# Performance work log

Measured on AMD Instinct MI355X. Metric: run time of the kernel, lower is better.

## Reference

```python
import jax, jax.numpy as jnp
import numpy as np
from jax import lax

K = 15            # contrast_kernel
BRIGHT_T = 0.7    # brightness_threshold

def _box_filter(x, k):
    # x: [B,1,H,W]; uniform k x k conv with SAME (zero) padding, matching F.conv2d(padding=k//2)
    kernel = jnp.full((1, 1, k, k), 1.0 / (k * k), dtype=x.dtype)
    pad = k // 2
    return lax.conv_general_dilated(
        x, kernel, window_strides=(1, 1), padding=[(pad, pad), (pad, pad)],
        dimension_numbers=('NCHW', 'OIHW', 'NCHW'))

def _avg_pool_5x5(x):
    # avg_pool2d(kernel=5, stride=1, padding=2), count_include_pad=True (torch default)
    s = lax.reduce_window(x, jnp.array(0.0, x.dtype), lax.add,
                          window_dimensions=(1, 1, 5, 5), window_strides=(1, 1, 1, 1),
                          padding=[(0, 0), (0, 0), (2, 2), (2, 2)])
    return s / jnp.array(25.0, x.dtype)

def setup_inputs() -> dict:
    key = jax.random.key(0)
    img = jax.random.uniform(key, (16, 3, 1024, 1024), dtype=jnp.float32)
    return {"img": img}

def reference(img) -> jnp.ndarray:
    # luminance: [B,1,H,W]
    lum = (0.299 * img[:, 0:1] + 0.587 * img[:, 1:2] + 0.114 * img[:, 2:3])
    brightness_mask = jax.nn.sigmoid((lum - BRIGHT_T) * 10.0)
    local_mean = _box_filter(lum, K)
    local_var = _box_filter((lum - local_mean) ** 2, K)
    contrast_mask = jax.nn.sigmoid(local_var * 50.0 - 0.5)
    max_rgb = jnp.max(img, axis=1, keepdims=True)
    min_rgb = jnp.min(img, axis=1, keepdims=True)
    saturation = (max_rgb - min_rgb) / (max_rgb + 1e-8)
    low_sat_mask = jax.nn.sigmoid((0.3 - saturation) * 10.0)
    combined = jnp.clip(brightness_mask + 0.5 * contrast_mask * low_sat_mask, 0.0, 1.0)
    return _avg_pool_5x5(combined)
```

## Files before the change

kernel.cpp:

```cpp
#include <hip/hip_runtime.h>


#define BLOCK 512
typedef unsigned short u16;
typedef unsigned int u32;
typedef __attribute__((ext_vector_type(2))) float f32x2;

#define SL 104
#define S1 88

__device__ __forceinline__ float blo(u32 u){ return __uint_as_float(u << 16); }
__device__ __forceinline__ float bhi(u32 u){ return __uint_as_float(u & 0xffff0000u); }
__device__ __forceinline__ u32 pk2(float lo, float hi){
    u32 r; asm("v_cvt_pk_bf16_f32 %0, %1, %2" : "=v"(r) : "v"(lo), "v"(hi)); return r;
}
__device__ __forceinline__ f32x2 pka(f32x2 a, f32x2 b){
    f32x2 d; asm("v_pk_add_f32 %0, %1, %2" : "=v"(d) : "v"(a), "v"(b)); return d;
}
__device__ __forceinline__ f32x2 up2(u32 u){
    f32x2 r; r.x = __uint_as_float(u << 16); r.y = __uint_as_float(u & 0xffff0000u); return r;
}
__device__ __forceinline__ float sigf(float x){ return 1.f / (1.f + __expf(-x)); }
__device__ __forceinline__ float clamp01(float x){ return fminf(fmaxf(x, 0.f), 1.f); }
__device__ __forceinline__ void unp8(uint4 v, float* o){
    o[0]=blo(v.x); o[1]=bhi(v.x); o[2]=blo(v.y); o[3]=bhi(v.y);
    o[4]=blo(v.z); o[5]=bhi(v.z); o[6]=blo(v.w); o[7]=bhi(v.w);
}
__device__ __forceinline__ float satm(float r_, float g_, float b_){
    float mx = fmaxf(r_, fmaxf(g_, b_));
    float mn = fminf(r_, fminf(g_, b_));
    float sat = (mx - mn) / (mx + 1e-8f);
    return sigf((0.3f - sat) * 10.f);
}

template<bool EDGE>
__device__ __forceinline__ void body(const float* __restrict__ pR,
                                     const float* __restrict__ pG,
                                     const float* __restrict__ pB,
                                     float* __restrict__ po,
                                     int oy, int ox, int tid,
                                     u16* sLum, u16* sT1, u16* sDC)
{
    const float C225 = 1.f / 225.f;
    const float CF   = 50.f / 225.f;

    for (int task = tid; task < 96 * 6; task += BLOCK) {
        int r = task / 6, c = task - r * 6;
        int gy = oy - 16 + r;
        int gxb = ox - 16 + 16 * c;
        u32 pk[8];
        #pragma unroll
        for (int sq = 0; sq < 4; ++sq) {
            int gx = gxb + 4 * sq;
            float l0 = 0.f, l1 = 0.f, l2 = 0.f, l3 = 0.f;
            if (!EDGE || ((unsigned)gy < 1024u && (unsigned)gx < 1024u)) {
                int idx = gy * 1024 + gx;
                float4 R  = *(const float4*)&pR[idx];
                float4 G  = *(const float4*)&pG[idx];
                float4 Bc = *(const float4*)&pB[idx];
                l0 = fmaf(0.299f, R.x, fmaf(0.587f, G.x, 0.114f * Bc.x));
                l1 = fmaf(0.299f, R.y, fmaf(0.587f, G.y, 0.114f * Bc.y));
                l2 = fmaf(0.299f, R.z, fmaf(0.587f, G.z, 0.114f * Bc.z));
                l3 = fmaf(0.299f, R.w, fmaf(0.587f, G.w, 0.114f * Bc.w));
            }
            pk[2 * sq]     = pk2(l0, l1);
            pk[2 * sq + 1] = pk2(l2, l3);
        }
        u16* dst = &sLum[r * SL + 16 * c];
        *(uint4*)dst     = make_uint4(pk[0], pk[1], pk[2], pk[3]);
        *(uint4*)(dst+8) = make_uint4(pk[4], pk[5], pk[6], pk[7]);
    }
    __syncthreads();

    for (int task = tid; task < 96 * 6; task += BLOCK) {
        int r = task / 6, g = task - r * 6;
        int s0 = 16 * g;
        const u16* lr = &sLum[r * SL + s0];
        float lv[32];
        unp8(*(const uint4*)lr,        lv);
        unp8(*(const uint4*)(lr + 8),  lv + 8);
        unp8(*(const uint4*)(lr + 16), lv + 16);
        unp8(*(const uint4*)(lr + 24), lv + 24);
        float o[16];
        float s = 0.f;
        #pragma unroll
        for (int k = 0; k < 15; ++k) s += lv[k];
        o[0] = s;
        #pragma unroll
        for (int j = 1; j < 16; ++j) { s += lv[j + 14] - lv[j - 1]; o[j] = s; }
        u16* dst = &sT1[r * S1 + s0];
        if (g < 5) {
            *(uint4*)dst     = make_uint4(pk2(o[0],o[1]), pk2(o[2],o[3]),
                                          pk2(o[4],o[5]), pk2(o[6],o[7]));
            *(uint4*)(dst+8) = make_uint4(pk2(o[8],o[9]),  pk2(o[10],o[11]),
                                          pk2(o[12],o[13]),pk2(o[14],o[15]));
        } else {
            *(uint2*)dst = make_uint2(pk2(o[0],o[1]), pk2(o[2],o[3]));
        }
    }
    __syncthreads();

    for (int task = tid; task < 451; task += BLOCK) {
        int rg = task / 11, cg = task - rg * 11;
        int r0 = 2 * rg, c0 = 8 * cg;
        const u16* hp = &sT1[r0 * S1 + c0];
        f32x2 a0, a1, a2, a3, cs0, cs1, cs2, cs3;
        {
            uint4 v = *(const uint4*)hp;
            a0 = up2(v.x); a1 = up2(v.y); a2 = up2(v.z); a3 = up2(v.w);
        }
        {
            uint4 v = *(const uint4*)(hp + S1);
            cs0 = up2(v.x); cs1 = up2(v.y); cs2 = up2(v.z); cs3 = up2(v.w);
        }
        #pragma unroll
        for (int k = 2; k <= 14; ++k) {
            uint4 v = *(const uint4*)(hp + k * S1);
            cs0 = pka(cs0, up2(v.x)); cs1 = pka(cs1, up2(v.y));
            cs2 = pka(cs2, up2(v.z)); cs3 = pka(cs3, up2(v.w));
        }
        auto emitD = [&](int row, f32x2 t0, f32x2 t1, f32x2 t2, f32x2 t3) {
            const u16* lrow = &sLum[(row + 7) * SL + c0];
            u32 aw  = *(const u32*)(lrow + 6);
            uint4 bv = *(const uint4*)(lrow + 8);
            float L0 = bhi(aw);
            float L1 = blo(bv.x), L2 = bhi(bv.x);
            float L3 = blo(bv.y), L4 = bhi(bv.y);
            float L5 = blo(bv.z), L6 = bhi(bv.z);
            float L7 = blo(bv.w);
            float t_0 = fmaf(-C225, t0.x, L0), t_1 = fmaf(-C225, t0.y, L1);
            float t_2 = fmaf(-C225, t1.x, L2), t_3 = fmaf(-C225, t1.y, L3);
            float t_4 = fmaf(-C225, t2.x, L4), t_5 = fmaf(-C225, t2.y, L5);
            float t_6 = fmaf(-C225, t3.x, L6), t_7 = fmaf(-C225, t3.y, L7);
            float d0=t_0*t_0, d1=t_1*t_1, d2=t_2*t_2, d3=t_3*t_3;
            float d4=t_4*t_4, d5=t_5*t_5, d6=t_6*t_6, d7=t_7*t_7;
            if (EDGE) {
                int gy = oy - 9 + row, gx = ox - 9 + c0;
                bool vy = (unsigned)gy < 1024u;
                d0 = (vy && (unsigned)(gx    ) < 1024u) ? d0 : 0.f;
                d1 = (vy && (unsigned)(gx + 1) < 1024u) ? d1 : 0.f;
                d2 = (vy && (unsigned)(gx + 2) < 1024u) ? d2 : 0.f;
                d3 = (vy && (unsigned)(gx + 3) < 1024u) ? d3 : 0.f;
                d4 = (vy && (unsigned)(gx + 4) < 1024u) ? d4 : 0.f;
                d5 = (vy && (unsigned)(gx + 5) < 1024u) ? d5 : 0.f;
                d6 = (vy && (unsigned)(gx + 6) < 1024u) ? d6 : 0.f;
                d7 = (vy && (unsigned)(gx + 7) < 1024u) ? d7 : 0.f;
            }
            *(uint4*)&sDC[row * S1 + c0] =
                make_uint4(pk2(d0,d1), pk2(d2,d3), pk2(d4,d5), pk2(d6,d7));
        };
        emitD(r0, pka(cs0,a0), pka(cs1,a1), pka(cs2,a2), pka(cs3,a3));
        {
            uint4 v = *(const uint4*)(hp + 15 * S1);
            emitD(r0 + 1, pka(cs0, up2(v.x)), pka(cs1, up2(v.y)),
                          pka(cs2, up2(v.z)), pka(cs3, up2(v.w)));
        }
    }
    __syncthreads();

    for (int task = tid; task < 82 * 5; task += BLOCK) {
        int r = task / 5, g = task - r * 5;
        int s0 = 16 * g;
        const u16* dr = &sDC[r * S1 + s0];
        float lv[32];
        unp8(*(const uint4*)dr,        lv);
        unp8(*(const uint4*)(dr + 8),  lv + 8);
        unp8(*(const uint4*)(dr + 16), lv + 16);
        unp8(*(const uint4*)(dr + 24), lv + 24);
        float o[16];
        float s = 0.f;
        #pragma unroll
        for (int k = 0; k < 15; ++k) s += lv[k];
        o[0] = s;
        #pragma unroll
        for (int j = 1; j < 16; ++j) { s += lv[j + 14] - lv[j - 1]; o[j] = s; }
        u16* dst = &sT1[r * S1 + s0];
        if (g < 4) {
            *(uint4*)dst     = make_uint4(pk2(o[0],o[1]), pk2(o[2],o[3]),
                                          pk2(o[4],o[5]), pk2(o[6],o[7]));
            *(uint4*)(dst+8) = make_uint4(pk2(o[8],o[9]),  pk2(o[10],o[11]),
                                          pk2(o[12],o[13]),pk2(o[14],o[15]));
        } else {
            *(uint2*)dst = make_uint2(pk2(o[0],o[1]), pk2(o[2],o[3]));
        }
    }
    __syncthreads();

    for (int task = tid; task < 289; task += BLOCK) {
        int rg = task / 17, q = task - rg * 17;
        int r0 = 4 * rg, c0 = 4 * q;
        const u16* hp = &sT1[r0 * S1 + c0];
        f32x2 cs0, cs1, n00,n01, n10,n11, n20,n21;
        {
            uint2 v = *(const uint2*)hp;
            cs0 = up2(v.x); cs1 = up2(v.y);
            n00 = -cs0; n01 = -cs1;
        }
        {
            uint2 v = *(const uint2*)(hp + S1);
            f32x2 e0 = up2(v.x), e1 = up2(v.y);
            n10 = -e0; n11 = -e1;
            cs0 = pka(cs0, e0); cs1 = pka(cs1, e1);
        }
        {
            uint2 v = *(const uint2*)(hp + 2 * S1);
            f32x2 e0 = up2(v.x), e1 = up2(v.y);
            n20 = -e0; n21 = -e1;
            cs0 = pka(cs0, e0); cs1 = pka(cs1, e1);
        }
        #pragma unroll
        for (int k = 3; k < 15; ++k) {
            uint2 v = *(const uint2*)(hp + k * S1);
            cs0 = pka(cs0, up2(v.x)); cs1 = pka(cs1, up2(v.y));
        }
        auto emitC = [&](int row) {
            float cm0 = sigf(fmaf(cs0.x, CF, -0.5f));
            float cm1 = sigf(fmaf(cs0.y, CF, -0.5f));
            float cm2 = sigf(fmaf(cs1.x, CF, -0.5f));
            float cm3 = sigf(fmaf(cs1.y, CF, -0.5f));
            const u16* lr = &sLum[(row + 14) * SL + c0 + 14];
            u32 la = *(const u32*)lr;
            u32 lb = *(const u32*)(lr + 2);
            float bm0 = sigf((blo(la) - 0.7f) * 10.f);
            float bm1 = sigf((bhi(la) - 0.7f) * 10.f);
            float bm2 = sigf((blo(lb) - 0.7f) * 10.f);
            float bm3 = sigf((bhi(lb) - 0.7f) * 10.f);
            int gy = oy - 2 + row, gx0 = ox - 2 + c0;
            int i0 = gy * 1024 + gx0;
            float2 z2 = make_float2(0.f, 0.f);
            float2 Ra, Rb, Ga, Gb, Ba, Bb;
            bool va = true, vb = true;
            if (EDGE) {
                bool vy = (unsigned)gy < 1024u;
                va = vy && (unsigned)gx0 < 1024u;
                vb = vy && (unsigned)(gx0 + 2) < 1024u;
                Ra = va ? *(const float2*)&pR[i0]     : z2;
                Rb = vb ? *(const float2*)&pR[i0 + 2] : z2;
                Ga = va ? *(const float2*)&pG[i0]     : z2;
                Gb = vb ? *(const float2*)&pG[i0 + 2] : z2;
                Ba = va ? *(const float2*)&pB[i0]     : z2;
                Bb = vb ? *(const float2*)&pB[i0 + 2] : z2;
            } else {
                Ra = *(const float2*)&pR[i0];  Rb = *(const float2*)&pR[i0 + 2];
                Ga = *(const float2*)&pG[i0];  Gb = *(const float2*)&pG[i0 + 2];
                Ba = *(const float2*)&pB[i0];  Bb = *(const float2*)&pB[i0 + 2];
            }
            float cb0 = clamp01(bm0 + 0.5f * cm0 * satm(Ra.x, Ga.x, Ba.x));
            float cb1 = clamp01(bm1 + 0.5f * cm1 * satm(Ra.y, Ga.y, Ba.y));
            float cb2 = clamp01(bm2 + 0.5f * cm2 * satm(Rb.x, Gb.x, Bb.x));
            float cb3 = clamp01(bm3 + 0.5f * cm3 * satm(Rb.y, Gb.y, Bb.y));
            if (EDGE) {
                cb0 = va ? cb0 : 0.f;  cb1 = va ? cb1 : 0.f;
                cb2 = vb ? cb2 : 0.f;  cb3 = vb ? cb3 : 0.f;
            }
            *(uint2*)&sDC[row * S1 + c0] = make_uint2(pk2(cb0,cb1), pk2(cb2,cb3));
        };
        emitC(r0);
        {
            uint2 v = *(const uint2*)(hp + 15 * S1);
            cs0 = pka(pka(cs0, up2(v.x)), n00); cs1 = pka(pka(cs1, up2(v.y)), n01);
        }
        emitC(r0 + 1);
        {
            uint2 v = *(const uint2*)(hp + 16 * S1);
            cs0 = pka(pka(cs0, up2(v.x)), n10); cs1 = pka(pka(cs1, up2(v.y)), n11);
        }
        emitC(r0 + 2);
        {
            uint2 v = *(const uint2*)(hp + 17 * S1);
            cs0 = pka(pka(cs0, up2(v.x)), n20); cs1 = pka(pka(cs1, up2(v.y)), n21);
        }
        emitC(r0 + 3);
    }
    __syncthreads();

    for (int task = tid; task < 68 * 4; task += BLOCK) {
        int r = task >> 2, g = task & 3;
        int s0 = 16 * g;
        const u16* cr = &sDC[r * S1 + s0];
        float cv[24];
        unp8(*(const uint4*)cr,        cv);
        unp8(*(const uint4*)(cr + 8),  cv + 8);
        unp8(*(const uint4*)(cr + 16), cv + 16);
        float o[16];
        float s = cv[0] + cv[1] + cv[2] + cv[3] + cv[4];
        o[0] = s;
        #pragma unroll
        for (int j = 1; j < 16; ++j) { s += cv[j + 4] - cv[j - 1]; o[j] = s; }
        u16* dst = &sT1[r * S1 + s0];
        *(uint4*)dst = make_uint4(pk2(o[0], o[1]), pk2(o[2], o[3]),
                                  pk2(o[4], o[5]), pk2(o[6], o[7]));
        *(uint4*)(dst + 8) = make_uint4(pk2(o[8],  o[9]),  pk2(o[10], o[11]),
                                        pk2(o[12], o[13]), pk2(o[14], o[15]));
    }
    __syncthreads();

    for (int task = tid; task < 512; task += BLOCK) {
        int rg = task >> 4, q = task & 15;
        int r0 = 2 * rg, c0 = 4 * q;
        const u16* hp = &sT1[r0 * S1 + c0];
        f32x2 a0, a1, cs0, cs1;
        {
            uint2 v = *(const uint2*)hp;
            a0 = up2(v.x); a1 = up2(v.y);
        }
        {
            uint2 v = *(const uint2*)(hp + S1);
            cs0 = up2(v.x); cs1 = up2(v.y);
        }
        {
            uint2 v = *(const uint2*)(hp + 2 * S1);
            cs0 = pka(cs0, up2(v.x)); cs1 = pka(cs1, up2(v.y));
        }
        {
            uint2 v = *(const uint2*)(hp + 3 * S1);
            cs0 = pka(cs0, up2(v.x)); cs1 = pka(cs1, up2(v.y));
        }
        {
            uint2 v = *(const uint2*)(hp + 4 * S1);
            cs0 = pka(cs0, up2(v.x)); cs1 = pka(cs1, up2(v.y));
        }
        const float C25 = 1.f / 25.f;
        float* o0 = po + (size_t)(oy + r0) * 1024 + ox + c0;
        f32x2 t0 = pka(cs0, a0), t1 = pka(cs1, a1);
        *(float4*)o0 = make_float4(t0.x*C25, t0.y*C25, t1.x*C25, t1.y*C25);
        {
            uint2 v = *(const uint2*)(hp + 5 * S1);
            t0 = pka(cs0, up2(v.x)); t1 = pka(cs1, up2(v.y));
        }
        *(float4*)(o0 + 1024) = make_float4(t0.x*C25, t0.y*C25, t1.x*C25, t1.y*C25);
    }
}

__global__ __launch_bounds__(BLOCK, 6)
void wrd_kernel(const float* __restrict__ img, float* __restrict__ out) {
    __shared__ u16 sLum[96 * SL + 16];
    __shared__ u16 sT1[96 * S1];
    __shared__ u16 sDC[84 * S1 + 16];

    int bid = blockIdx.x, nwg = gridDim.x;
    int flat = ((nwg & 7) == 0) ? ((bid & 7) * (nwg >> 3) + (bid >> 3)) : bid;
    const int b = flat >> 8;
    const int t = flat & 255;
    const int oy = (t >> 4) * 64, ox = (t & 15) * 64;

    const float* pR = img + (size_t)b * 3145728u;
    const float* pG = pR + 1048576;
    const float* pB = pR + 2097152;
    float* po = out + (size_t)b * 1048576u;

    bool edge = (ox == 0) | (oy == 0) | (ox == 960) | (oy == 960);
    if (edge) body<true >(pR, pG, pB, po, oy, ox, threadIdx.x, sLum, sT1, sDC);
    else      body<false>(pR, pG, pB, po, oy, ox, threadIdx.x, sLum, sT1, sDC);
}

extern "C" void kernel_launch(void* const* d_in, const int* in_sizes, int n_in,
                              void* d_out, int out_size, void* d_ws, size_t ws_size,
                              hipStream_t stream) {
    const float* img = (const float*)d_in[0];
    float* out = (float*)d_out;
    int Bn = in_sizes[0] / (3 * 1024 * 1024);
    int nwg = Bn * 256;
    hipLaunchKernelGGL(wrd_kernel, dim3(nwg), dim3(BLOCK), 0, stream, img, out);
}
```

Baseline: 120.1 us.

## Compute first 15x15 box filter with MFMA banded-matrix multiplies

Replaces the scalar sliding-window horizontal and vertical passes of the local-mean box filter with two bf16 MFMA matrix products against a banded ones matrix built in shared memory. The mean result is transposed through sT1, and the variance step reads it back to build the squared deviations. The final 5x5 pool now uses a running vertical sum over four rows per thread. It adds a fourth shared buffer and lowers launch bounds occupancy from 6 to 4, doing redundant multiply-by-zero work in exchange for moving the reductions onto the matrix cores.

Measured after the change: 147.6 us. 22.9% more time.

```diff
diff --git a/kernel.cpp b/kernel.cpp
--- a/kernel.cpp
+++ b/kernel.cpp
@@ -5,12 +5,16 @@
 typedef unsigned short u16;
 typedef unsigned int u32;
 typedef __attribute__((ext_vector_type(2))) float f32x2;
+typedef __attribute__((ext_vector_type(4))) float f32x4;
+typedef __attribute__((ext_vector_type(8))) short bf16x8;
 
 #define SL 104
-#define S1 88
+#define ST 104
+#define SD 88
 
 __device__ __forceinline__ float blo(u32 u){ return __uint_as_float(u << 16); }
 __device__ __forceinline__ float bhi(u32 u){ return __uint_as_float(u & 0xffff0000u); }
+__device__ __forceinline__ float bf2f(u16 h){ return __uint_as_float(((u32)h) << 16); }
 __device__ __forceinline__ u32 pk2(float lo, float hi){
     u32 r; asm("v_cvt_pk_bf16_f32 %0, %1, %2" : "=v"(r) : "v"(lo), "v"(hi)); return r;
 }
@@ -31,6 +35,9 @@
     float mn = fminf(r_, fminf(g_, b_));
     float sat = (mx - mn) / (mx + 1e-8f);
     return sigf((0.3f - sat) * 10.f);
+}
+__device__ __forceinline__ f32x4 mf(bf16x8 a, bf16x8 b, f32x4 c){
+    return __builtin_amdgcn_mfma_f32_16x16x32_bf16(a, b, c, 0, 0, 0);
 }
 
 template<bool EDGE>
@@ -39,8 +46,10 @@
                                      const float* __restrict__ pB,
                                      float* __restrict__ po,
                                      int oy, int ox, int tid,
-                                     u16* sLum, u16* sT1, u16* sDC)
+                                     u16* sLum, u16* sBT, u16* sT1, u16* sDC)
 {
+    const int lane = tid & 63, wid = tid >> 6;
+    const int lrow = lane & 15, lgrp = lane >> 4;
     const float C225 = 1.f / 225.f;
     const float CF   = 50.f / 225.f;
 
@@ -70,126 +79,94 @@
         *(uint4*)dst     = make_uint4(pk[0], pk[1], pk[2], pk[3]);
         *(uint4*)(dst+8) = make_uint4(pk[4], pk[5], pk[6], pk[7]);
     }
-    __syncthreads();
-
-    for (int task = tid; task < 96 * 6; task += BLOCK) {
+    for (int idx = tid; idx < 96 * 12; idx += BLOCK) {
+        int a = idx / 12, c8 = idx - a * 12;
+        int b0 = 8 * c8;
+        u32 w[4];
+        #pragma unroll
+        for (int p = 0; p < 4; ++p) {
+            int b = b0 + 2 * p;
+            u32 lo = (b   >= a && b   <= a + 14) ? 0x3F80u : 0u;
+            u32 hi = (b+1 >= a && b+1 <= a + 14) ? 0x3F80u : 0u;
+            w[p] = lo | (hi << 16);
+        }
+        *(uint4*)&sBT[a * SL + b0] = make_uint4(w[0], w[1], w[2], w[3]);
+    }
+    __syncthreads();
+
+    for (int t = wid; t < 36; t += 8) {
+        int mt = t / 6, nt = t - mt * 6;
+        const u16* ap = &sLum[(mt * 16 + lrow) * SL + lgrp * 8];
+        const u16* bp = &sBT [(nt * 16 + lrow) * SL + lgrp * 8];
+        f32x4 acc = {0.f, 0.f, 0.f, 0.f};
+        acc = mf(*(const bf16x8*)ap,        *(const bf16x8*)bp,        acc);
+        acc = mf(*(const bf16x8*)(ap + 32), *(const bf16x8*)(bp + 32), acc);
+        acc = mf(*(const bf16x8*)(ap + 64), *(const bf16x8*)(bp + 64), acc);
+        int j = nt * 16 + lrow, i0 = mt * 16 + lgrp * 4;
+        bool jv = j < 82;
+        float h0 = jv ? acc[0] : 0.f, h1 = jv ? acc[1] : 0.f;
+        float h2 = jv ? acc[2] : 0.f, h3 = jv ? acc[3] : 0.f;
+        *(uint2*)&sT1[j * ST + i0] = make_uint2(pk2(h0, h1), pk2(h2, h3));
+    }
+    __syncthreads();
+
+    for (int t = wid; t < 36; t += 8) {
+        int mt = t / 6, nt = t - mt * 6;
+        const u16* ap = &sBT[(mt * 16 + lrow) * SL + lgrp * 8];
+        const u16* bp = &sT1[(nt * 16 + lrow) * ST + lgrp * 8];
+        f32x4 acc = {0.f, 0.f, 0.f, 0.f};
+        acc = mf(*(const bf16x8*)ap,        *(const bf16x8*)bp,        acc);
+        acc = mf(*(const bf16x8*)(ap + 32), *(const bf16x8*)(bp + 32), acc);
+        acc = mf(*(const bf16x8*)(ap + 64), *(const bf16x8*)(bp + 64), acc);
+        int j = nt * 16 + lrow, ib = mt * 16 + lgrp * 4;
+        int jc = min(j + 7, 95);
+        #pragma unroll
+        for (int r = 0; r < 4; ++r) {
+            int i = ib + r;
+            float mean = acc[r] * C225;
+            float l = bf2f(sLum[min(i + 7, 95) * SL + jc]);
+            float tt = l - mean;
+            float dv = tt * tt;
+            if (EDGE) {
+                int gy = oy - 9 + i, gx = ox - 9 + j;
+                if (!((unsigned)gy < 1024u && (unsigned)gx < 1024u)) dv = 0.f;
+            }
+            if (j < SD) sDC[i * SD + j] = (u16)pk2(dv, dv);
+        }
+    }
+    __syncthreads();
+
+    for (int task = tid; task < 82 * 6; task += BLOCK) {
         int r = task / 6, g = task - r * 6;
-        int s0 = 16 * g;
-        const u16* lr = &sLum[r * SL + s0];
-        float lv[32];
-        unp8(*(const uint4*)lr,        lv);
-        unp8(*(const uint4*)(lr + 8),  lv + 8);
-        unp8(*(const uint4*)(lr + 16), lv + 16);
-        unp8(*(const uint4*)(lr + 24), lv + 24);
-        float o[16];
-        float s = 0.f;
-        #pragma unroll
-        for (int k = 0; k < 15; ++k) s += lv[k];
-        o[0] = s;
-        #pragma unroll
-        for (int j = 1; j < 16; ++j) { s += lv[j + 14] - lv[j - 1]; o[j] = s; }
-        u16* dst = &sT1[r * S1 + s0];
-        if (g < 5) {
-            *(uint4*)dst     = make_uint4(pk2(o[0],o[1]), pk2(o[2],o[3]),
-                                          pk2(o[4],o[5]), pk2(o[6],o[7]));
-            *(uint4*)(dst+8) = make_uint4(pk2(o[8],o[9]),  pk2(o[10],o[11]),
-                                          pk2(o[12],o[13]),pk2(o[14],o[15]));
-        } else {
-            *(uint2*)dst = make_uint2(pk2(o[0],o[1]), pk2(o[2],o[3]));
-        }
-    }
-    __syncthreads();
-
-    for (int task = tid; task < 451; task += BLOCK) {
-        int rg = task / 11, cg = task - rg * 11;
-        int r0 = 2 * rg, c0 = 8 * cg;
-        const u16* hp = &sT1[r0 * S1 + c0];
-        f32x2 a0, a1, a2, a3, cs0, cs1, cs2, cs3;
-        {
-            uint4 v = *(const uint4*)hp;
-            a0 = up2(v.x); a1 = up2(v.y); a2 = up2(v.z); a3 = up2(v.w);
-        }
-        {
-            uint4 v = *(const uint4*)(hp + S1);
-            cs0 = up2(v.x); cs1 = up2(v.y); cs2 = up2(v.z); cs3 = up2(v.w);
-        }
-        #pragma unroll
-        for (int k = 2; k <= 14; ++k) {
-            uint4 v = *(const uint4*)(hp + k * S1);
-            cs0 = pka(cs0, up2(v.x)); cs1 = pka(cs1, up2(v.y));
-            cs2 = pka(cs2, up2(v.z)); cs3 = pka(cs3, up2(v.w));
-        }
-        auto emitD = [&](int row, f32x2 t0, f32x2 t1, f32x2 t2, f32x2 t3) {
-            const u16* lrow = &sLum[(row + 7) * SL + c0];
-            u32 aw  = *(const u32*)(lrow + 6);
-            uint4 bv = *(const uint4*)(lrow + 8);
-            float L0 = bhi(aw);
-            float L1 = blo(bv.x), L2 = bhi(bv.x);
-            float L3 = blo(bv.y), L4 = bhi(bv.y);
-            float L5 = blo(bv.z), L6 = bhi(bv.z);
-            float L7 = blo(bv.w);
-            float t_0 = fmaf(-C225, t0.x, L0), t_1 = fmaf(-C225, t0.y, L1);
-            float t_2 = fmaf(-C225, t1.x, L2), t_3 = fmaf(-C225, t1.y, L3);
-            float t_4 = fmaf(-C225, t2.x, L4), t_5 = fmaf(-C225, t2.y, L5);
-            float t_6 = fmaf(-C225, t3.x, L6), t_7 = fmaf(-C225, t3.y, L7);
-            float d0=t_0*t_0, d1=t_1*t_1, d2=t_2*t_2, d3=t_3*t_3;
-            float d4=t_4*t_4, d5=t_5*t_5, d6=t_6*t_6, d7=t_7*t_7;
-            if (EDGE) {
-                int gy = oy - 9 + row, gx = ox - 9 + c0;
-                bool vy = (unsigned)gy < 1024u;
-                d0 = (vy && (unsigned)(gx    ) < 1024u) ? d0 : 0.f;
-                d1 = (vy && (unsigned)(gx + 1) < 1024u) ? d1 : 0.f;
-                d2 = (vy && (unsigned)(gx + 2) < 1024u) ? d2 : 0.f;
-                d3 = (vy && (unsigned)(gx + 3) < 1024u) ? d3 : 0.f;
-                d4 = (vy && (unsigned)(gx + 4) < 1024u) ? d4 : 0.f;
-                d5 = (vy && (unsigned)(gx + 5) < 1024u) ? d5 : 0.f;
-                d6 = (vy && (unsigned)(gx + 6) < 1024u) ? d6 : 0.f;
-                d7 = (vy && (unsigned)(gx + 7) < 1024u) ? d7 : 0.f;
-            }
-            *(uint4*)&sDC[row * S1 + c0] =
-                make_uint4(pk2(d0,d1), pk2(d2,d3), pk2(d4,d5), pk2(d6,d7));
-        };
-        emitD(r0, pka(cs0,a0), pka(cs1,a1), pka(cs2,a2), pka(cs3,a3));
-        {
-            uint4 v = *(const uint4*)(hp + 15 * S1);
-            emitD(r0 + 1, pka(cs0, up2(v.x)), pka(cs1, up2(v.y)),
-                          pka(cs2, up2(v.z)), pka(cs3, up2(v.w)));
-        }
-    }
-    __syncthreads();
-
-    for (int task = tid; task < 82 * 5; task += BLOCK) {
-        int r = task / 5, g = task - r * 5;
-        int s0 = 16 * g;
-        const u16* dr = &sDC[r * S1 + s0];
+        int s0 = 12 * g, c0 = s0 & ~7;
+        const u16* dr = &sDC[r * SD + c0];
         float lv[32];
         unp8(*(const uint4*)dr,        lv);
         unp8(*(const uint4*)(dr + 8),  lv + 8);
         unp8(*(const uint4*)(dr + 16), lv + 16);
         unp8(*(const uint4*)(dr + 24), lv + 24);
-        float o[16];
+        if (s0 & 4) {
+            #pragma unroll
+            for (int i = 0; i < 28; ++i) lv[i] = lv[i + 4];
+        }
+        float o[12];
         float s = 0.f;
         #pragma unroll
         for (int k = 0; k < 15; ++k) s += lv[k];
         o[0] = s;
         #pragma unroll
-        for (int j = 1; j < 16; ++j) { s += lv[j + 14] - lv[j - 1]; o[j] = s; }
-        u16* dst = &sT1[r * S1 + s0];
-        if (g < 4) {
-            *(uint4*)dst     = make_uint4(pk2(o[0],o[1]), pk2(o[2],o[3]),
-                                          pk2(o[4],o[5]), pk2(o[6],o[7]));
-            *(uint4*)(dst+8) = make_uint4(pk2(o[8],o[9]),  pk2(o[10],o[11]),
-                                          pk2(o[12],o[13]),pk2(o[14],o[15]));
-        } else {
-            *(uint2*)dst = make_uint2(pk2(o[0],o[1]), pk2(o[2],o[3]));
-        }
+        for (int j = 1; j < 12; ++j) { s += lv[j + 14] - lv[j - 1]; o[j] = s; }
+        u16* dst = &sT1[r * ST + s0];
+        *(uint2*)dst       = make_uint2(pk2(o[0], o[1]),  pk2(o[2], o[3]));
+        *(uint2*)(dst + 4) = make_uint2(pk2(o[4], o[5]),  pk2(o[6], o[7]));
+        *(uint2*)(dst + 8) = make_uint2(pk2(o[8], o[9]),  pk2(o[10], o[11]));
     }
     __syncthreads();
 
     for (int task = tid; task < 289; task += BLOCK) {
         int rg = task / 17, q = task - rg * 17;
-        int r0 = 4 * rg, c0 = 4 * q;
-        const u16* hp = &sT1[r0 * S1 + c0];
+        int r0 = 4 * rg, c0v = 4 * q;
+        const u16* hp = &sT1[r0 * ST + c0v];
         f32x2 cs0, cs1, n00,n01, n10,n11, n20,n21;
         {
             uint2 v = *(const uint2*)hp;
@@ -197,20 +174,20 @@
             n00 = -cs0; n01 = -cs1;
         }
         {
-            uint2 v = *(const uint2*)(hp + S1);
+            uint2 v = *(const uint2*)(hp + ST);
             f32x2 e0 = up2(v.x), e1 = up2(v.y);
             n10 = -e0; n11 = -e1;
             cs0 = pka(cs0, e0); cs1 = pka(cs1, e1);
         }
         {
-            uint2 v = *(const uint2*)(hp + 2 * S1);
+            uint2 v = *(const uint2*)(hp + 2 * ST);
             f32x2 e0 = up2(v.x), e1 = up2(v.y);
             n20 = -e0; n21 = -e1;
             cs0 = pka(cs0, e0); cs1 = pka(cs1, e1);
         }
         #pragma unroll
         for (int k = 3; k < 15; ++k) {
-            uint2 v = *(const uint2*)(hp + k * S1);
+            uint2 v = *(const uint2*)(hp + k * ST);
             cs0 = pka(cs0, up2(v.x)); cs1 = pka(cs1, up2(v.y));
         }
         auto emitC = [&](int row) {
@@ -218,14 +195,14 @@
             float cm1 = sigf(fmaf(cs0.y, CF, -0.5f));
             float cm2 = sigf(fmaf(cs1.x, CF, -0.5f));
             float cm3 = sigf(fmaf(cs1.y, CF, -0.5f));
-            const u16* lr = &sLum[(row + 14) * SL + c0 + 14];
-            u32 la = *(const u32*)lr;
-            u32 lb = *(const u32*)(lr + 2);
-            float bm0 = sigf((blo(la) - 0.7f) * 10.f);
-            float bm1 = sigf((bhi(la) - 0.7f) * 10.f);
-            float bm2 = sigf((blo(lb) - 0.7f) * 10.f);
-            float bm3 = sigf((bhi(lb) - 0.7f) * 10.f);
-            int gy = oy - 2 + row, gx0 = ox - 2 + c0;
+            const u16* lp = &sLum[(row + 14) * SL + c0v + 12];
+            ushort4 A  = *(const ushort4*)lp;
+            ushort4 Bv = *(const ushort4*)(lp + 4);
+            float bm0 = sigf((bf2f(A.z)  - 0.7f) * 10.f);
+            float bm1 = sigf((bf2f(A.w)  - 0.7f) * 10.f);
+            float bm2 = sigf((bf2f(Bv.x) - 0.7f) * 10.f);
+            float bm3 = sigf((bf2f(Bv.y) - 0.7f) * 10.f);
+            int gy = oy - 2 + row, gx0 = ox - 2 + c0v;
             int i0 = gy * 1024 + gx0;
             float2 z2 = make_float2(0.f, 0.f);
             float2 Ra, Rb, Ga, Gb, Ba, Bb;
@@ -253,21 +230,21 @@
                 cb0 = va ? cb0 : 0.f;  cb1 = va ? cb1 : 0.f;
                 cb2 = vb ? cb2 : 0.f;  cb3 = vb ? cb3 : 0.f;
             }
-            *(uint2*)&sDC[row * S1 + c0] = make_uint2(pk2(cb0,cb1), pk2(cb2,cb3));
+            *(uint2*)&sDC[row * SD + c0v] = make_uint2(pk2(cb0,cb1), pk2(cb2,cb3));
         };
         emitC(r0);
         {
-            uint2 v = *(const uint2*)(hp + 15 * S1);
+            uint2 v = *(const uint2*)(hp + 15 * ST);
             cs0 = pka(pka(cs0, up2(v.x)), n00); cs1 = pka(pka(cs1, up2(v.y)), n01);
         }
         emitC(r0 + 1);
         {
-            uint2 v = *(const uint2*)(hp + 16 * S1);
+            uint2 v = *(const uint2*)(hp + 16 * ST);
             cs0 = pka(pka(cs0, up2(v.x)), n10); cs1 = pka(pka(cs1, up2(v.y)), n11);
         }
         emitC(r0 + 2);
         {
-            uint2 v = *(const uint2*)(hp + 17 * S1);
+            uint2 v = *(const uint2*)(hp + 17 * ST);
             cs0 = pka(pka(cs0, up2(v.x)), n20); cs1 = pka(pka(cs1, up2(v.y)), n21);
         }
         emitC(r0 + 3);
@@ -277,7 +254,7 @@
     for (int task = tid; task < 68 * 4; task += BLOCK) {
         int r = task >> 2, g = task & 3;
         int s0 = 16 * g;
-        const u16* cr = &sDC[r * S1 + s0];
+        const u16* cr = &sDC[r * SD + s0];
         float cv[24];
         unp8(*(const uint4*)cr,        cv);
         unp8(*(const uint4*)(cr + 8),  cv + 8);
@@ -287,7 +264,7 @@
         o[0] = s;
         #pragma unroll
         for (int j = 1; j < 16; ++j) { s += cv[j + 4] - cv[j - 1]; o[j] = s; }
-        u16* dst = &sT1[r * S1 + s0];
+        u16* dst = &sT1[r * ST + s0];
         *(uint4*)dst = make_uint4(pk2(o[0], o[1]), pk2(o[2], o[3]),
                                   pk2(o[4], o[5]), pk2(o[6], o[7]));
         *(uint4*)(dst + 8) = make_uint4(pk2(o[8],  o[9]),  pk2(o[10], o[11]),
@@ -295,48 +272,49 @@
     }
     __syncthreads();
 
-    for (int task = tid; task < 512; task += BLOCK) {
+    for (int task = tid; task < 256; task += BLOCK) {
         int rg = task >> 4, q = task & 15;
-        int r0 = 2 * rg, c0 = 4 * q;
-        const u16* hp = &sT1[r0 * S1 + c0];
-        f32x2 a0, a1, cs0, cs1;
-        {
-            uint2 v = *(const uint2*)hp;
-            a0 = up2(v.x); a1 = up2(v.y);
-        }
-        {
-            uint2 v = *(const uint2*)(hp + S1);
-            cs0 = up2(v.x); cs1 = up2(v.y);
-        }
-        {
-            uint2 v = *(const uint2*)(hp + 2 * S1);
-            cs0 = pka(cs0, up2(v.x)); cs1 = pka(cs1, up2(v.y));
-        }
-        {
-            uint2 v = *(const uint2*)(hp + 3 * S1);
-            cs0 = pka(cs0, up2(v.x)); cs1 = pka(cs1, up2(v.y));
-        }
-        {
-            uint2 v = *(const uint2*)(hp + 4 * S1);
-            cs0 = pka(cs0, up2(v.x)); cs1 = pka(cs1, up2(v.y));
+        int r0 = 4 * rg, c0v = 4 * q;
+        const u16* hp = &sT1[r0 * ST + c0v];
+        f32x2 cs0, cs1, a00, a01, a10, a11, a20, a21;
+        #pragma unroll
+        for (int k = 0; k < 5; ++k) {
+            uint2 v = *(const uint2*)(hp + k * ST);
+            f32x2 x0 = up2(v.x), x1 = up2(v.y);
+            if (k == 0) { cs0 = x0; cs1 = x1; a00 = x0; a01 = x1; }
+            else {
+                if (k == 1) { a10 = x0; a11 = x1; }
+                if (k == 2) { a20 = x0; a21 = x1; }
+                cs0 = pka(cs0, x0); cs1 = pka(cs1, x1);
+            }
         }
         const float C25 = 1.f / 25.f;
-        float* o0 = po + (size_t)(oy + r0) * 1024 + ox + c0;
-        f32x2 t0 = pka(cs0, a0), t1 = pka(cs1, a1);
-        *(float4*)o0 = make_float4(t0.x*C25, t0.y*C25, t1.x*C25, t1.y*C25);
-        {
-            uint2 v = *(const uint2*)(hp + 5 * S1);
-            t0 = pka(cs0, up2(v.x)); t1 = pka(cs1, up2(v.y));
-        }
-        *(float4*)(o0 + 1024) = make_float4(t0.x*C25, t0.y*C25, t1.x*C25, t1.y*C25);
-    }
-}
-
-__global__ __launch_bounds__(BLOCK, 6)
+        float* o0 = po + (size_t)(oy + r0) * 1024 + ox + c0v;
+        *(float4*)o0 = make_float4(cs0.x*C25, cs0.y*C25, cs1.x*C25, cs1.y*C25);
+        {
+            uint2 v = *(const uint2*)(hp + 5 * ST);
+            cs0 = pka(pka(cs0, up2(v.x)), -a00); cs1 = pka(pka(cs1, up2(v.y)), -a01);
+        }
+        *(float4*)(o0 + 1024) = make_float4(cs0.x*C25, cs0.y*C25, cs1.x*C25, cs1.y*C25);
+        {
+            uint2 v = *(const uint2*)(hp + 6 * ST);
+            cs0 = pka(pka(cs0, up2(v.x)), -a10); cs1 = pka(pka(cs1, up2(v.y)), -a11);
+        }
+        *(float4*)(o0 + 2048) = make_float4(cs0.x*C25, cs0.y*C25, cs1.x*C25, cs1.y*C25);
+        {
+            uint2 v = *(const uint2*)(hp + 7 * ST);
+            cs0 = pka(pka(cs0, up2(v.x)), -a20); cs1 = pka(pka(cs1, up2(v.y)), -a21);
+        }
+        *(float4*)(o0 + 3072) = make_float4(cs0.x*C25, cs0.y*C25, cs1.x*C25, cs1.y*C25);
+    }
+}
+
+__global__ __launch_bounds__(BLOCK, 4)
 void wrd_kernel(const float* __restrict__ img, float* __restrict__ out) {
     __shared__ u16 sLum[96 * SL + 16];
-    __shared__ u16 sT1[96 * S1];
-    __shared__ u16 sDC[84 * S1 + 16];
+    __shared__ u16 sBT [96 * SL];
+    __shared__ u16 sT1 [96 * ST];
+    __shared__ u16 sDC [96 * SD];
 
     int bid = blockIdx.x, nwg = gridDim.x;
     int flat = ((nwg & 7) == 0) ? ((bid & 7) * (nwg >> 3) + (bid >> 3)) : bid;
@@ -350,8 +328,8 @@
     float* po = out + (size_t)b * 1048576u;
 
     bool edge = (ox == 0) | (oy == 0) | (ox == 960) | (oy == 960);
-    if (edge) body<true >(pR, pG, pB, po, oy, ox, threadIdx.x, sLum, sT1, sDC);
-    else      body<false>(pR, pG, pB, po, oy, ox, threadIdx.x, sLum, sT1, sDC);
+    if (edge) body<true >(pR, pG, pB, po, oy, ox, threadIdx.x, sLum, sBT, sT1, sDC);
+    else      body<false>(pR, pG, pB, po, oy, ox, threadIdx.x, sLum, sBT, sT1, sDC);
 }
 
 extern "C" void kernel_launch(void* const* d_in, const int* in_sizes, int n_in,
```
